# Kernel optimization log

Hardware: AMD Instinct MI355X
Metric: run time of the kernel (lower is better)

The kernel has to match this reference:

```python
import jax, jax.numpy as jnp
import numpy as np

N, C, T, V = 32, 64, 512, 25
CO = 64            # out_channels
C4 = CO // 4       # inter channel (conv_a/conv_d output, kc//3)
W3 = 3 * V         # unfolded node dim
BN_EPS = 1e-5


def setup_inputs() -> dict:
    key = jax.random.key(0)
    ks = jax.random.split(key, 12)
    s = 0.05
    return {
        "x": jax.random.normal(ks[0], (N, C, T, V), dtype=jnp.float32),
        "A": jax.random.uniform(ks[1], (3, W3, W3), dtype=jnp.float32) * 0.1,  # fixed adjacency buffer
        "PA": jnp.full((3, W3, W3), 1e-6, dtype=jnp.float32),                   # learned adjacency offset
        "conv_a_w": jax.random.normal(ks[2], (C4, C), dtype=jnp.float32) * s,   # 1x1 conv_a[0]
        "conv_a_b": jnp.zeros((C4,), dtype=jnp.float32),
        "conv_d_w": jax.random.normal(ks[3], (C4, C), dtype=jnp.float32) * s,   # 1x1 conv_d[0]
        "conv_d_b": jnp.zeros((C4,), dtype=jnp.float32),
        "conv_w": jax.random.normal(ks[4], (3 * C4, C), dtype=jnp.float32) * s, # main 1x1 conv (t_kernel_size=1)
        "conv_b": jnp.zeros((3 * C4,), dtype=jnp.float32),
        "out_w": jax.random.normal(ks[5], (CO, C4, 3), dtype=jnp.float32) * s,  # conv3d kernel (1,3,1)
        "out_b": jnp.zeros((CO,), dtype=jnp.float32),
        "bn_gamma": jnp.ones((CO,), dtype=jnp.float32),
        "bn_beta": jnp.zeros((CO,), dtype=jnp.float32),
        "bn_mean": jnp.zeros((CO,), dtype=jnp.float32),
        "bn_var": jnp.ones((CO,), dtype=jnp.float32),
    }


def _unfold3(x):
    # UnfoldTemporalWindows(3,1,1): (N,C,T,V) -> (N,C,T,3V), zero-pad T by 1
    n, c, t, v = x.shape
    xp = jnp.pad(x, ((0, 0), (0, 0), (1, 1), (0, 0)))
    win = jnp.stack([xp[:, :, i:i + t, :] for i in range(3)], axis=3)  # (N,C,T,3,V)
    return win.reshape(n, c, t, 3 * v)


def reference(x, A, PA, conv_a_w, conv_a_b, conv_d_w, conv_d_b,
              conv_w, conv_b, out_w, out_b, bn_gamma, bn_beta, bn_mean, bn_var):
    n, c, t, v = x.shape
    w3 = 3 * v
    Aeff = A + PA  # (3, 3V, 3V)

    x2 = _unfold3(x)  # (N,C,T,3V)

    # adaptive graph attention: matmul-softmax-matmul
    a1 = jnp.einsum('nctw,oc->notw', x2, conv_a_w) + conv_a_b[None, :, None, None]  # (N,C4,T,3V)
    a11 = a1.transpose(0, 3, 1, 2).reshape(n, w3, -1)   # (N,3V,C4*T)
    a2 = a1.reshape(n, -1, w3)                          # (N,C4*T,3V)
    att = jax.nn.softmax(jnp.matmul(a11, a2) / w3, axis=-2)  # (N,3V,3V), softmax over dim -2
    xz = jnp.matmul(x2.reshape(n, c * t, w3), att).reshape(n, c, t, w3)
    z = jnp.einsum('nctw,oc->notw', xz, conv_d_w) + conv_d_b[None, :, None, None]  # (N,C4,T,3V)

    # main branch: 1x1 conv -> split into k=3 -> einsum graph conv with A
    x1 = jnp.einsum('nctw,oc->notw', x2, conv_w) + conv_b[None, :, None, None]  # (N,3*C4,T,3V)
    c4 = conv_d_w.shape[0]
    x1 = x1.reshape(n, 3, c4, t, w3)
    x1 = jnp.einsum('nkctv,kvw->nctw', x1, Aeff)  # (N,C4,T,3V)
    x1 = x1 + z

    # conv3d (1,3,1) collapses the window-of-3 dim
    x1 = x1.reshape(n, c4, t, 3, v)
    y = jnp.einsum('nctwv,ocw->notv', x1, out_w) + out_b[None, :, None, None]  # (N,CO,T,V)

    # BatchNorm2d (inference form)
    inv = jax.lax.rsqrt(bn_var + BN_EPS)
    y = (y - bn_mean[None, :, None, None]) * (bn_gamma * inv)[None, :, None, None] + bn_beta[None, :, None, None]

    y = y + x  # in_channels == out_channels -> identity residual
    return jax.nn.relu(y)
```

## Files before the change

kernel.cpp:

```cpp
#include <hip/hip_runtime.h>
#include <hip/hip_bf16.h>


typedef unsigned short u16;
typedef unsigned int   u32;
typedef __attribute__((ext_vector_type(8))) short bf16x8;
typedef __attribute__((ext_vector_type(4))) float f32x4;

__device__ __forceinline__ float b2f(u32 u) {
    union { u32 i; float f; } x; x.i = (u & 0xffffu) << 16; return x.f;
}
__device__ __forceinline__ u16 f2b(float f) {
    union { float f; u32 i; } x; x.f = f;
    u32 i = x.i;
    return (u16)((i + 0x7fffu + ((i >> 16) & 1u)) >> 16);
}
__device__ __forceinline__ u32 pack2(float a, float b) {
    return (u32)f2b(a) | ((u32)f2b(b) << 16);
}

__global__ __launch_bounds__(256) void k0_bta(
    const float* __restrict__ A, const float* __restrict__ PA,
    u16* __restrict__ BtA)
{
    int e = blockIdx.x * 256 + threadIdx.x;
    if (e >= 80 * 288) return;
    int w = e / 288, k = e - w * 288;
    int r = k >> 5, v = k & 31, g = r / 3, i = r - g * 3;
    float val = 0.f;
    if (v < 25 && w < 75) {
        int idx = (g * 75 + i * 25 + v) * 75 + w;
        val = A[idx] + PA[idx];
    }
    BtA[e] = f2b(val);
}

__global__ __launch_bounds__(256, 2) void k1_conv80(
    const float* __restrict__ x,
    const float* __restrict__ wa, const float* __restrict__ ba,
    const float* __restrict__ wd, const float* __restrict__ bd,
    const float* __restrict__ wc, const float* __restrict__ bc,
    u16* __restrict__ a1o, u16* __restrict__ hcn)
{
    __shared__ __align__(16) u16 Xt[256 * 64];
    __shared__ __align__(16) u16 Csh[80 * 264];
    char* XtB = (char*)Xt;

    const int b    = blockIdx.x;
    const int n    = b >> 4;
    const int t0   = (b & 15) << 5;
    const int tid  = threadIdx.x;
    const int wave = tid >> 6, lane = tid & 63;
    const int q    = lane >> 4, r = lane & 15;

    bf16x8 wfrag[5][2];
    float  breg[5];
    #pragma unroll
    for (int mt = 0; mt < 5; ++mt) {
        const int o = mt * 16 + r;
        const float* src = (o < 16) ? (wa + o * 64)
                         : (o < 32) ? (wd + (o - 16) * 64)
                                    : (wc + (o - 32) * 64);
        breg[mt] = (o < 16) ? ba[o] : (o < 32) ? bd[o - 16] : bc[o - 32];
        #pragma unroll
        for (int ks = 0; ks < 2; ++ks) {
            bf16x8 f;
            #pragma unroll
            for (int j = 0; j < 8; ++j)
                f[j] = (short)f2b(src[ks * 32 + q * 8 + j]);
            wfrag[mt][ks] = f;
        }
    }

    if (t0 == 0) {
        uint4 z; z.x = 0u; z.y = 0u; z.z = 0u; z.w = 0u;
        for (int e = tid; e < 50; e += 256)
            *(uint4*)&a1o[((size_t)n * 514) * 400 + e * 8] = z;
    }
    if (t0 == 480) {
        uint4 z; z.x = 0u; z.y = 0u; z.z = 0u; z.w = 0u;
        for (int e = tid; e < 50; e += 256)
            *(uint4*)&a1o[((size_t)n * 514 + 513) * 400 + e * 8] = z;
    }

    {
        uint4 z; z.x = 0u; z.y = 0u; z.z = 0u; z.w = 0u;
        for (int e = tid; e < 448; e += 256) {
            const int pc = e >> 3, ch = e & 7;
            const int tl = pc / 7, pv = pc - tl * 7;
            const int col = tl * 32 + 25 + pv;
            *(uint4*)(XtB + col * 128 + ch * 16) = z;
        }
    }

    auto epilogue = [&](int tbp) {
        for (int e = tid; e < 2048; e += 256) {
            const int cc  = e >> 5;
            const int rem = e & 31;
            const int tl  = rem >> 2, v0 = (rem & 3) << 3;
            const int o   = (cc < 48) ? cc + 32 : cc - 32;
            uint4 pk = *(const uint4*)&Csh[o * 264 + tl * 32 + v0];
            *(uint4*)&hcn[(((size_t)n * 64 + cc) * 512 + (tbp + tl)) * 32 + v0] = pk;
        }
        for (int e = tid; e < 400; e += 256) {
            const int tv = e >> 1, h = (e & 1) << 3;
            const int tl = (tv * 41) >> 10;
            const int v  = tv - tl * 25;
            const int cb = tl * 32 + v;
            u16 a[8];
            #pragma unroll
            for (int k = 0; k < 8; ++k) a[k] = Csh[(h + k) * 264 + cb];
            uint4 pk;
            pk.x = (u32)a[0] | ((u32)a[1] << 16);
            pk.y = (u32)a[2] | ((u32)a[3] << 16);
            pk.z = (u32)a[4] | ((u32)a[5] << 16);
            pk.w = (u32)a[6] | ((u32)a[7] << 16);
            *(uint4*)&a1o[(((size_t)n * 514 + (tbp + tl + 1)) * 25 + v) * 16 + h] = pk;
        }
    };

    for (int s = 0; s < 4; ++s) {
        const int tb = t0 + s * 8;

        if (s > 0) epilogue(tb - 8);
        for (int e = tid; e < 400; e += 256) {
            const int co = e / 50;
            const int tq = e - co * 50;
            const float* gp = x + (((size_t)n * 64 + co * 8) * 512 + tb) * 25 + tq * 4;
            float fl[32];
            #pragma unroll
            for (int i = 0; i < 8; ++i) {
                const float4 t4 = *(const float4*)(gp + (size_t)i * 12800);
                fl[i * 4 + 0] = t4.x; fl[i * 4 + 1] = t4.y;
                fl[i * 4 + 2] = t4.z; fl[i * 4 + 3] = t4.w;
            }
            #pragma unroll
            for (int j = 0; j < 4; ++j) {
                const int tv  = tq * 4 + j;
                const int tl  = (tv * 41) >> 10;
                const int col = tl * 32 + (tv - tl * 25);
                uint4 pk;
                pk.x = pack2(fl[0 * 4 + j], fl[1 * 4 + j]);
                pk.y = pack2(fl[2 * 4 + j], fl[3 * 4 + j]);
                pk.z = pack2(fl[4 * 4 + j], fl[5 * 4 + j]);
                pk.w = pack2(fl[6 * 4 + j], fl[7 * 4 + j]);
                *(uint4*)(XtB + col * 128 + ((co * 16) ^ ((col & 7) << 4))) = pk;
            }
        }
        __syncthreads();

        {
            f32x4 acc[4][5];
            #pragma unroll
            for (int a_ = 0; a_ < 4; ++a_)
                #pragma unroll
                for (int m_ = 0; m_ < 5; ++m_)
                    acc[a_][m_] = (f32x4){0.f, 0.f, 0.f, 0.f};

            #pragma unroll
            for (int nt4 = 0; nt4 < 4; ++nt4) {
                const int col = (wave * 4 + nt4) * 16 + r;
                const int swz = (col & 7) << 4;
                const char* rowp = (const char*)Xt + col * 128;
                const bf16x8 x0 = *(const bf16x8*)(rowp + ((q * 16) ^ swz));
                const bf16x8 x1 = *(const bf16x8*)(rowp + ((64 + q * 16) ^ swz));
                #pragma unroll
                for (int mt = 0; mt < 5; ++mt) {
                    acc[nt4][mt] = __builtin_amdgcn_mfma_f32_16x16x32_bf16(
                        x0, wfrag[mt][0], acc[nt4][mt], 0, 0, 0);
                    acc[nt4][mt] = __builtin_amdgcn_mfma_f32_16x16x32_bf16(
                        x1, wfrag[mt][1], acc[nt4][mt], 0, 0, 0);
                }
            }
            #pragma unroll
            for (int nt4 = 0; nt4 < 4; ++nt4) {
                const int colb = (wave * 4 + nt4) * 16 + q * 4;
                #pragma unroll
                for (int mt = 0; mt < 5; ++mt) {
                    const int o = mt * 16 + r;
                    const float bi = breg[mt];
                    uint2 pr;
                    pr.x = pack2(acc[nt4][mt][0] + bi, acc[nt4][mt][1] + bi);
                    pr.y = pack2(acc[nt4][mt][2] + bi, acc[nt4][mt][3] + bi);
                    *(uint2*)&Csh[o * 264 + colb] = pr;
                }
            }
        }
        __syncthreads();
    }
    epilogue(t0 + 24);
}

__global__ __launch_bounds__(256, 2) void k2a_mfma(
    const u16* __restrict__ a1o, float* __restrict__ Spart)
{
    __shared__ u16 U[80 * 136];
    __shared__ float Sred[80 * 80];
    const int b   = blockIdx.x;
    const int n   = b >> 4;
    const int tc  = b & 15;
    const int t0  = tc * 32;
    const int tid = threadIdx.x;
    const int wave = tid >> 6, lane = tid & 63;
    const int q = lane >> 4, col = lane & 15;

    f32x4 acc[25];
    #pragma unroll
    for (int i = 0; i < 25; ++i) acc[i] = (f32x4){0.f, 0.f, 0.f, 0.f};

    for (int s = 0; s < 4; ++s) {
        __syncthreads();
        for (int e = tid; e < 1280; e += 256) {
            int row = e >> 4, c8 = (e & 15) << 3;
            uint4 val; val.x = 0u; val.y = 0u; val.z = 0u; val.w = 0u;
            if (row < 75) {
                int i = row / 25, v = row - i * 25;
                int tl = c8 >> 4, o0 = c8 & 8;
                int tp = t0 + s * 8 + tl + i;
                val = *(const uint4*)&a1o[(((size_t)n * 514 + tp) * 25 + v) * 16 + o0];
            }
            *(uint4*)&U[row * 136 + c8] = val;
        }
        __syncthreads();

        const int k0 = wave * 32 + q * 8;
        bf16x8 fr[5];
        #pragma unroll
        for (int r = 0; r < 5; ++r)
            fr[r] = *(const bf16x8*)&U[(r * 16 + col) * 136 + k0];
        #pragma unroll
        for (int mt = 0; mt < 5; ++mt)
            #pragma unroll
            for (int nt = 0; nt < 5; ++nt)
                acc[mt * 5 + nt] = __builtin_amdgcn_mfma_f32_16x16x32_bf16(
                    fr[mt], fr[nt], acc[mt * 5 + nt], 0, 0, 0);
    }

    for (int w = 0; w < 4; ++w) {
        if (wave == w) {
            #pragma unroll
            for (int mt = 0; mt < 5; ++mt)
                #pragma unroll
                for (int nt = 0; nt < 5; ++nt)
                    #pragma unroll
                    for (int reg = 0; reg < 4; ++reg) {
                        int idx = (mt * 16 + q * 4 + reg) * 80 + nt * 16 + col;
                        if (w == 0) Sred[idx]  = acc[mt * 5 + nt][reg];
                        else        Sred[idx] += acc[mt * 5 + nt][reg];
                    }
        }
        __syncthreads();
    }
    float* dst = &Spart[(size_t)(n * 16 + tc) * 6400];
    for (int e = tid; e < 6400; e += 256) dst[e] = Sred[e];
}

__global__ __launch_bounds__(256) void k2b_softmax(
    const float* __restrict__ Spart, u16* __restrict__ BtT)
{
    __shared__ float S[6400];
    const int n = blockIdx.x, tid = threadIdx.x;
    for (int e = tid; e < 6400; e += 256) {
        float s = 0.f;
        for (int ks = 0; ks < 16; ++ks)
            s += Spart[(size_t)(n * 16 + ks) * 6400 + e];
        S[e] = s * (1.0f / 75.0f);
    }
    __syncthreads();
    if (tid < 80) {
        const int w2 = tid;
        float r = 0.f;
        if (w2 < 75) {
            float m = -1e30f;
            for (int w1 = 0; w1 < 75; ++w1) m = fmaxf(m, S[w1 * 80 + w2]);
            float s = 0.f;
            for (int w1 = 0; w1 < 75; ++w1) {
                float e = __expf(S[w1 * 80 + w2] - m);
                S[w1 * 80 + w2] = e;
                s += e;
            }
            r = 1.0f / s;
        }
        for (int k = 0; k < 96; ++k) {
            int i = k >> 5, v = k & 31;
            float val = (w2 < 75 && v < 25) ? S[(i * 25 + v) * 80 + w2] * r : 0.f;
            BtT[((size_t)n * 80 + w2) * 96 + k] = f2b(val);
        }
    }
}

__global__ __launch_bounds__(256, 2) void k3_graph(
    const u16* __restrict__ hcn, const u16* __restrict__ BtA,
    const u16* __restrict__ BtT, u16* __restrict__ sum12)
{
    __shared__ u16 Bt[80 * 392];
    const int b    = blockIdx.x;
    const int n    = b >> 4;
    const int tblk = (b & 15) << 5;
    const int tid  = threadIdx.x;

    for (int e = tid; e < 3840; e += 256) {
        int row = e / 48, cs = e - row * 48;
        uint4 val;
        if (cs < 36) val = *(const uint4*)&BtA[row * 288 + cs * 8];
        else         val = *(const uint4*)&BtT[((size_t)n * 80 + row) * 96 + (cs - 36) * 8];
        *(uint4*)&Bt[row * 392 + cs * 8] = val;
    }
    __syncthreads();

    const int wave = tid >> 6, lane = tid & 63;
    const int c = lane & 15, q = lane >> 4;
    const int tb = tblk + wave * 8;

    for (int tt = 0; tt < 8; tt += 2) {
        const int t0 = tb + tt, t1 = t0 + 1;
        bf16x8 a0[12], a1[12];
        #pragma unroll
        for (int r = 0; r < 12; ++r) {
            const int g = r / 3, i = r - g * 3;
            const size_t rowb = ((size_t)n * 64 + g * 16 + c) * 512;
            const int tp0 = t0 + i - 1, tp1 = t1 + i - 1;
            a0[r] = (tp0 >= 0 && tp0 < 512)
                  ? *(const bf16x8*)&hcn[(rowb + tp0) * 32 + q * 8] : (bf16x8)(short)0;
            a1[r] = (tp1 >= 0 && tp1 < 512)
                  ? *(const bf16x8*)&hcn[(rowb + tp1) * 32 + q * 8] : (bf16x8)(short)0;
        }
        #pragma unroll 1
        for (int nt = 0; nt < 5; ++nt) {
            f32x4 acc0 = {0.f, 0.f, 0.f, 0.f};
            f32x4 acc1 = {0.f, 0.f, 0.f, 0.f};
            const u16* bp = &Bt[(nt * 16 + c) * 392 + q * 8];
            #pragma unroll
            for (int r = 0; r < 12; ++r) {
                bf16x8 bf = *(const bf16x8*)(bp + r * 32);
                acc0 = __builtin_amdgcn_mfma_f32_16x16x32_bf16(bf, a0[r], acc0, 0, 0, 0);
                acc1 = __builtin_amdgcn_mfma_f32_16x16x32_bf16(bf, a1[r], acc1, 0, 0, 0);
            }
            const size_t tb0 = ((size_t)n * 512 + t0) * 1200;
            const size_t tb1 = ((size_t)n * 512 + t1) * 1200;
            #pragma unroll
            for (int reg = 0; reg < 4; ++reg) {
                const int w = nt * 16 + q * 4 + reg;
                if (w < 75) {
                    const int ww = (w >= 50) ? 2 : ((w >= 25) ? 1 : 0);
                    const int v  = w - ww * 25;
                    const int off = (v * 3 + ww) * 16 + c;
                    sum12[tb0 + off] = f2b(acc0[reg]);
                    sum12[tb1 + off] = f2b(acc1[reg]);
                }
            }
        }
    }
}

__global__ __launch_bounds__(256, 3) void k4_out(
    const u16* __restrict__ sum12,
    const float* __restrict__ ow, const float* __restrict__ obias,
    const float* __restrict__ bg, const float* __restrict__ bb,
    const float* __restrict__ bm, const float* __restrict__ bv,
    const float* __restrict__ x, float* __restrict__ out)
{
    __shared__ __align__(16) char smem[64 * 204 * 4];
    u16*   Bsh = (u16*)smem;
    float* Csh = (float*)smem;
    char*  BshB = smem;

    const int b    = blockIdx.x;
    const int n    = b >> 6;
    const int t0   = (b & 63) << 3;
    const int tid  = threadIdx.x;
    const int wave = tid >> 6, lane = tid & 63;
    const int q    = lane >> 4, c15 = lane & 15;

    {
        uint4 z; z.x = 0u; z.y = 0u; z.z = 0u; z.w = 0u;
        for (int e = tid; e < 960; e += 256) {
            int col, j;
            if (e < 512) { col = e >> 1; j = 6 + (e & 1); }
            else {
                const int r2 = e - 512;
                const int cc = r2 >> 3; j = r2 & 7;
                const int tl = cc / 7, pv = cc - tl * 7;
                col = tl * 32 + 25 + pv;
            }
            *(uint4*)(BshB + col * 128 + ((j * 16) ^ ((col & 7) << 4))) = z;
        }
    }
    for (int e = tid; e < 1200; e += 256) {
        const int j  = e % 6;
        const int rv = e / 6;
        const int tl = (rv * 41) >> 10;
        const int v  = rv - tl * 25;
        const uint4 val = *(const uint4*)
            &sum12[((size_t)n * 512 + t0 + tl) * 1200 + v * 48 + j * 8];
        const int col = tl * 32 + v;
        *(uint4*)(BshB + col * 128 + ((j * 16) ^ ((col & 7) << 4))) = val;
    }

    bf16x8 wfrag[4][2];
    #pragma unroll
    for (int mt = 0; mt < 4; ++mt) {
        const int o = mt * 16 + c15;
        #pragma unroll
        for (int ks = 0; ks < 2; ++ks) {
            bf16x8 f;
            #pragma unroll
            for (int j = 0; j < 8; ++j) {
                const int k = ks * 32 + q * 8 + j;
                const int cc = k & 15, ww = k >> 4;
                f[j] = (k < 48) ? (short)f2b(ow[o * 48 + cc * 3 + ww]) : (short)0;
            }
            wfrag[mt][ks] = f;
        }
    }
    float scl[4][4], shf2[4][4];
    #pragma unroll
    for (int mt = 0; mt < 4; ++mt)
        #pragma unroll
        for (int reg = 0; reg < 4; ++reg) {
            const int o = mt * 16 + q * 4 + reg;
            const float s = bg[o] * rsqrtf(bv[o] + 1e-5f);
            scl[mt][reg]  = s;
            shf2[mt][reg] = bb[o] + (obias[o] - bm[o]) * s;
        }
    __syncthreads();

    f32x4 acc[4][4];
    #pragma unroll
    for (int ct = 0; ct < 4; ++ct)
        #pragma unroll
        for (int mt = 0; mt < 4; ++mt)
            acc[ct][mt] = (f32x4){0.f, 0.f, 0.f, 0.f};

    const int wb = wave * 64;
    #pragma unroll
    for (int ct = 0; ct < 4; ++ct) {
        const int col = wb + ct * 16 + c15;
        const int swz = (col & 7) << 4;
        const char* rp = BshB + col * 128;
        const bf16x8 b0 = *(const bf16x8*)(rp + ((q * 16) ^ swz));
        const bf16x8 b1 = *(const bf16x8*)(rp + ((64 + q * 16) ^ swz));
        #pragma unroll
        for (int mt = 0; mt < 4; ++mt) {
            acc[ct][mt] = __builtin_amdgcn_mfma_f32_16x16x32_bf16(
                wfrag[mt][0], b0, acc[ct][mt], 0, 0, 0);
            acc[ct][mt] = __builtin_amdgcn_mfma_f32_16x16x32_bf16(
                wfrag[mt][1], b1, acc[ct][mt], 0, 0, 0);
        }
    }
    __syncthreads();

    #pragma unroll
    for (int ct = 0; ct < 4; ++ct) {
        const int col = wb + ct * 16 + c15;
        const int tl = col >> 5, v = col & 31;
        if (v < 25) {
            const int cc = tl * 25 + v;
            #pragma unroll
            for (int mt = 0; mt < 4; ++mt)
                #pragma unroll
                for (int reg = 0; reg < 4; ++reg) {
                    const int o = mt * 16 + q * 4 + reg;
                    Csh[o * 204 + cc] =
                        acc[ct][mt][reg] * scl[mt][reg] + shf2[mt][reg];
                }
        }
    }
    __syncthreads();

    for (int e = tid; e < 3200; e += 256) {
        const int o = e / 50, jj = e - o * 50;
        const size_t gidx = (((size_t)n * 64 + o) * 512 + t0) * 25 + jj * 4;
        const float4 xv = *(const float4*)&x[gidx];
        const float* cp = &Csh[o * 204 + jj * 4];
        float4 yv;
        yv.x = fmaxf(cp[0] + xv.x, 0.f);
        yv.y = fmaxf(cp[1] + xv.y, 0.f);
        yv.z = fmaxf(cp[2] + xv.z, 0.f);
        yv.w = fmaxf(cp[3] + xv.w, 0.f);
        *(float4*)&out[gidx] = yv;
    }
}

extern "C" void kernel_launch(void* const* d_in, const int* in_sizes, int n_in,
                              void* d_out, int out_size, void* d_ws, size_t ws_size,
                              hipStream_t stream)
{
    const float* x  = (const float*)d_in[0];
    const float* A  = (const float*)d_in[1];
    const float* PA = (const float*)d_in[2];
    const float* wa = (const float*)d_in[3];
    const float* ba = (const float*)d_in[4];
    const float* wd = (const float*)d_in[5];
    const float* bd = (const float*)d_in[6];
    const float* wc = (const float*)d_in[7];
    const float* bc = (const float*)d_in[8];
    const float* ow = (const float*)d_in[9];
    const float* ob = (const float*)d_in[10];
    const float* bg = (const float*)d_in[11];
    const float* bb = (const float*)d_in[12];
    const float* bm = (const float*)d_in[13];
    const float* bv = (const float*)d_in[14];
    float* out = (float*)d_out;

    char* ws = (char*)d_ws;
    u16*   a1o   = (u16*)(ws);
    u16*   hcn   = (u16*)(ws + 13158400);
    u16*   sum12 = (u16*)(ws + 80267264);
    float* Spart = (float*)(ws + 80267264);
    u16*   BtA   = (u16*)(ws + 130598912);
    u16*   BtT   = (u16*)(ws + 130644992);

    k0_bta    <<<90,   256, 0, stream>>>(A, PA, BtA);
    k1_conv80 <<<512,  256, 0, stream>>>(x, wa, ba, wd, bd, wc, bc, a1o, hcn);
    k2a_mfma  <<<512,  256, 0, stream>>>(a1o, Spart);
    k2b_softmax<<<32,  256, 0, stream>>>(Spart, BtT);
    k3_graph  <<<512,  256, 0, stream>>>(hcn, BtA, BtT, sum12);
    k4_out    <<<2048, 256, 0, stream>>>(sum12, ow, ob, bg, bb, bm, bv, x, out);
}
```

Before: 449.1 us.

## Parallelize softmax across 160 blocks and halve k4 output tile

The softmax kernel previously used 32 blocks with only 80 active threads each. It now splits each batch into 5 column groups of 16, reduces partials into a small padded LDS tile, and does max/sum with 16-lane shuffles so all 256 threads work. The output kernel now handles 4 timesteps per block instead of 8, which halves LDS and accumulators so 5 blocks fit per CU and doubles the grid. This raises parallelism and occupancy, at the cost of more blocks and some repeated per-block weight and BN setup.

Measured after the change: 493.7 us. +9.9%, slower.

```diff
diff --git a/kernel.cpp b/kernel.cpp
--- a/kernel.cpp
+++ b/kernel.cpp
@@ -258,34 +258,45 @@
 __global__ __launch_bounds__(256) void k2b_softmax(
     const float* __restrict__ Spart, u16* __restrict__ BtT)
 {
-    __shared__ float S[6400];
-    const int n = blockIdx.x, tid = threadIdx.x;
-    for (int e = tid; e < 6400; e += 256) {
+    __shared__ float S2[75][17];
+    const int b = blockIdx.x;
+    const int n = b / 5, w2g = b - n * 5;
+    const int w2base = w2g * 16;
+    const int tid = threadIdx.x;
+
+    for (int e = tid; e < 1200; e += 256) {
+        const int w1 = e >> 4, w2l = e & 15;
+        const float* sp = &Spart[(size_t)(n * 16) * 6400 + w1 * 80 + w2base + w2l];
         float s = 0.f;
-        for (int ks = 0; ks < 16; ++ks)
-            s += Spart[(size_t)(n * 16 + ks) * 6400 + e];
-        S[e] = s * (1.0f / 75.0f);
+        #pragma unroll
+        for (int ks = 0; ks < 16; ++ks) s += sp[(size_t)ks * 6400];
+        S2[w1][w2l] = s * (1.0f / 75.0f);
     }
     __syncthreads();
-    if (tid < 80) {
-        const int w2 = tid;
-        float r = 0.f;
-        if (w2 < 75) {
-            float m = -1e30f;
-            for (int w1 = 0; w1 < 75; ++w1) m = fmaxf(m, S[w1 * 80 + w2]);
-            float s = 0.f;
-            for (int w1 = 0; w1 < 75; ++w1) {
-                float e = __expf(S[w1 * 80 + w2] - m);
-                S[w1 * 80 + w2] = e;
-                s += e;
-            }
-            r = 1.0f / s;
-        }
-        for (int k = 0; k < 96; ++k) {
-            int i = k >> 5, v = k & 31;
-            float val = (w2 < 75 && v < 25) ? S[(i * 25 + v) * 80 + w2] * r : 0.f;
-            BtT[((size_t)n * 80 + w2) * 96 + k] = f2b(val);
-        }
+
+    const int w2l = tid >> 4, j = tid & 15;
+    float m = -1e30f;
+    for (int w1 = j; w1 < 75; w1 += 16) m = fmaxf(m, S2[w1][w2l]);
+    #pragma unroll
+    for (int off = 8; off; off >>= 1) m = fmaxf(m, __shfl_xor(m, off, 16));
+    float s = 0.f;
+    for (int w1 = j; w1 < 75; w1 += 16) {
+        const float e = __expf(S2[w1][w2l] - m);
+        S2[w1][w2l] = e;
+        s += e;
+    }
+    #pragma unroll
+    for (int off = 8; off; off >>= 1) s += __shfl_xor(s, off, 16);
+    const float r = 1.0f / s;
+    for (int w1 = j; w1 < 75; w1 += 16) S2[w1][w2l] *= r;
+    __syncthreads();
+
+    for (int e = tid; e < 1536; e += 256) {
+        const int wl = e / 96, k = e - wl * 96;
+        const int i = k >> 5, v = k & 31;
+        const int w2 = w2base + wl;
+        const float val = (w2 < 75 && v < 25) ? S2[i * 25 + v][wl] : 0.f;
+        BtT[((size_t)n * 80 + w2) * 96 + k] = f2b(val);
     }
 }
 
@@ -353,32 +364,31 @@
     }
 }
 
-__global__ __launch_bounds__(256, 3) void k4_out(
+__global__ __launch_bounds__(256, 5) void k4_out(
     const u16* __restrict__ sum12,
     const float* __restrict__ ow, const float* __restrict__ obias,
     const float* __restrict__ bg, const float* __restrict__ bb,
     const float* __restrict__ bm, const float* __restrict__ bv,
     const float* __restrict__ x, float* __restrict__ out)
 {
-    __shared__ __align__(16) char smem[64 * 204 * 4];
-    u16*   Bsh = (u16*)smem;
-    float* Csh = (float*)smem;
+    __shared__ __align__(16) char smem[64 * 108 * 4];
+    float* Csh  = (float*)smem;
     char*  BshB = smem;
 
     const int b    = blockIdx.x;
-    const int n    = b >> 6;
-    const int t0   = (b & 63) << 3;
+    const int n    = b >> 7;
+    const int t0   = (b & 127) << 2;
     const int tid  = threadIdx.x;
     const int wave = tid >> 6, lane = tid & 63;
     const int q    = lane >> 4, c15 = lane & 15;
 
     {
         uint4 z; z.x = 0u; z.y = 0u; z.z = 0u; z.w = 0u;
-        for (int e = tid; e < 960; e += 256) {
+        for (int e = tid; e < 480; e += 256) {
             int col, j;
-            if (e < 512) { col = e >> 1; j = 6 + (e & 1); }
+            if (e < 256) { col = e >> 1; j = 6 + (e & 1); }
             else {
-                const int r2 = e - 512;
+                const int r2 = e - 256;
                 const int cc = r2 >> 3; j = r2 & 7;
                 const int tl = cc / 7, pv = cc - tl * 7;
                 col = tl * 32 + 25 + pv;
@@ -386,7 +396,7 @@
             *(uint4*)(BshB + col * 128 + ((j * 16) ^ ((col & 7) << 4))) = z;
         }
     }
-    for (int e = tid; e < 1200; e += 256) {
+    for (int e = tid; e < 600; e += 256) {
         const int j  = e % 6;
         const int rv = e / 6;
         const int tl = (rv * 41) >> 10;
@@ -425,16 +435,16 @@
         }
     __syncthreads();
 
-    f32x4 acc[4][4];
-    #pragma unroll
-    for (int ct = 0; ct < 4; ++ct)
+    f32x4 acc[2][4];
+    #pragma unroll
+    for (int ct = 0; ct < 2; ++ct)
         #pragma unroll
         for (int mt = 0; mt < 4; ++mt)
             acc[ct][mt] = (f32x4){0.f, 0.f, 0.f, 0.f};
 
-    const int wb = wave * 64;
-    #pragma unroll
-    for (int ct = 0; ct < 4; ++ct) {
+    const int wb = wave * 32;
+    #pragma unroll
+    for (int ct = 0; ct < 2; ++ct) {
         const int col = wb + ct * 16 + c15;
         const int swz = (col & 7) << 4;
         const char* rp = BshB + col * 128;
@@ -451,7 +461,7 @@
     __syncthreads();
 
     #pragma unroll
-    for (int ct = 0; ct < 4; ++ct) {
+    for (int ct = 0; ct < 2; ++ct) {
         const int col = wb + ct * 16 + c15;
         const int tl = col >> 5, v = col & 31;
         if (v < 25) {
@@ -461,18 +471,18 @@
                 #pragma unroll
                 for (int reg = 0; reg < 4; ++reg) {
                     const int o = mt * 16 + q * 4 + reg;
-                    Csh[o * 204 + cc] =
+                    Csh[o * 108 + cc] =
                         acc[ct][mt][reg] * scl[mt][reg] + shf2[mt][reg];
                 }
         }
     }
     __syncthreads();
 
-    for (int e = tid; e < 3200; e += 256) {
-        const int o = e / 50, jj = e - o * 50;
+    for (int e = tid; e < 1600; e += 256) {
+        const int o = e / 25, jj = e - o * 25;
         const size_t gidx = (((size_t)n * 64 + o) * 512 + t0) * 25 + jj * 4;
         const float4 xv = *(const float4*)&x[gidx];
-        const float* cp = &Csh[o * 204 + jj * 4];
+        const float* cp = &Csh[o * 108 + jj * 4];
         float4 yv;
         yv.x = fmaxf(cp[0] + xv.x, 0.f);
         yv.y = fmaxf(cp[1] + xv.y, 0.f);
@@ -514,7 +524,7 @@
     k0_bta    <<<90,   256, 0, stream>>>(A, PA, BtA);
     k1_conv80 <<<512,  256, 0, stream>>>(x, wa, ba, wd, bd, wc, bc, a1o, hcn);
     k2a_mfma  <<<512,  256, 0, stream>>>(a1o, Spart);
-    k2b_softmax<<<32,  256, 0, stream>>>(Spart, BtT);
+    k2b_softmax<<<160, 256, 0, stream>>>(Spart, BtT);
     k3_graph  <<<512,  256, 0, stream>>>(hcn, BtA, BtT, sum12);
-    k4_out    <<<2048, 256, 0, stream>>>(sum12, ow, ob, bg, bb, bm, bv, x, out);
-}
+    k4_out    <<<4096, 256, 0, stream>>>(sum12, ow, ob, bg, bb, bm, bv, x, out);
+}
```
